# Optimization experiments

Measured on AMD Instinct MI355X. Metric: run time of the kernel, lower is better.

Reference implementation:

```python
import jax, jax.numpy as jnp
import numpy as np

NUM_POSES = 4096
NUM_PATCHES = 262144
NUM_OBS = 2097152


def setup_inputs() -> dict:
    key = jax.random.key(0)
    ks = jax.random.split(key, 7)
    poses = jax.random.normal(ks[0], (NUM_POSES, 7), dtype=jnp.float32)
    patch_coords = jax.random.normal(ks[1], (NUM_PATCHES, 2), dtype=jnp.float32)
    elevation_angle = jax.random.normal(ks[2], (NUM_PATCHES, 1), dtype=jnp.float32)
    poses_idx = jax.random.randint(ks[3], (NUM_OBS,), 0, NUM_POSES)
    patch_idx = jax.random.randint(ks[4], (NUM_OBS,), 0, NUM_PATCHES)
    target_coords = jax.random.normal(ks[5], (NUM_OBS, 3), dtype=jnp.float32)
    weights = jax.random.uniform(ks[6], (NUM_OBS, 1), dtype=jnp.float32)
    return {
        "poses": poses,
        "patch_coords": patch_coords,
        "elevation_angle": elevation_angle,
        "poses_idx": poses_idx,
        "patch_idx": patch_idx,
        "target_coords": target_coords,
        "weights": weights,
    }


def _se3_apply(pose7, pts):
    # pose7: [M,7] = (tx,ty,tz,qx,qy,qz,qw); pts: [M,3]
    # Equivalent to transform_matrix(pose) @ [pts; 1] (rotation by unit quaternion + translation)
    t = pose7[:, :3]
    q = pose7[:, 3:]
    q = q / jnp.linalg.norm(q, axis=-1, keepdims=True)  # pp.SE3 keeps unit quats
    qv, qw = q[:, :3], q[:, 3:4]
    uv = jnp.cross(qv, pts)                     # [M,3]
    rotated = pts + 2.0 * (qw * uv + jnp.cross(qv, uv))
    return rotated + t


def _cart2polar(xyz):
    # (x,y,z) -> (range, azimuth, elevation)
    x, y, z = xyz[:, 0], xyz[:, 1], xyz[:, 2]
    rho = jnp.sqrt(x * x + y * y)
    r = jnp.sqrt(rho * rho + z * z)
    az = jnp.arctan2(y, x)
    el = jnp.arctan2(z, rho)
    return jnp.stack([r, az, el], axis=1)


def reference(poses, patch_coords, elevation_angle, poses_idx, patch_idx, target_coords, weights):
    p = poses[poses_idx]                                            # [M,7] gather
    pts = jnp.concatenate(
        [patch_coords[patch_idx], elevation_angle[patch_idx]], axis=1
    )                                                               # [M,3] gather+cat
    proj = _cart2polar(_se3_apply(p, pts))                          # [M,3]
    residual = (proj - target_coords) * weights                     # [M,3]
    return residual
```

## Files before the change

kernel.cpp:

```cpp
#include <hip/hip_runtime.h>
#include <hip/hip_bf16.h>


__global__ __launch_bounds__(256) void ba_residual_kernel(
    const float* __restrict__ poses,
    const float* __restrict__ patch_coords,
    const float* __restrict__ elev,
    const int*   __restrict__ poses_idx,
    const int*   __restrict__ patch_idx,
    const float* __restrict__ target,
    const float* __restrict__ weights,
    float*       __restrict__ out,
    int n4)
{
    int i4 = blockIdx.x * blockDim.x + threadIdx.x;
    if (i4 >= n4) return;

    int4   pidx = reinterpret_cast<const int4*>(poses_idx)[i4];
    int4   qidx = reinterpret_cast<const int4*>(patch_idx)[i4];
    float4 w4   = reinterpret_cast<const float4*>(weights)[i4];
    float4 t0   = reinterpret_cast<const float4*>(target)[i4 * 3 + 0];
    float4 t1   = reinterpret_cast<const float4*>(target)[i4 * 3 + 1];
    float4 t2   = reinterpret_cast<const float4*>(target)[i4 * 3 + 2];

    int   pi[4] = {pidx.x, pidx.y, pidx.z, pidx.w};
    int   qi[4] = {qidx.x, qidx.y, qidx.z, qidx.w};
    float ww[4] = {w4.x, w4.y, w4.z, w4.w};
    float tg[12] = {t0.x, t0.y, t0.z, t0.w,
                    t1.x, t1.y, t1.z, t1.w,
                    t2.x, t2.y, t2.z, t2.w};

    float res[12];

#pragma unroll
    for (int k = 0; k < 4; ++k) {
        const float* p = poses + (size_t)pi[k] * 7;
        float tx = p[0], ty = p[1], tz = p[2];
        float qx = p[3], qy = p[4], qz = p[5], qw = p[6];
        float inv = rsqrtf(qx*qx + qy*qy + qz*qz + qw*qw);
        qx *= inv; qy *= inv; qz *= inv; qw *= inv;

        float2 pc = *reinterpret_cast<const float2*>(patch_coords + (size_t)qi[k] * 2);
        float px = pc.x, py = pc.y, pz = elev[qi[k]];

        float ux = qy*pz - qz*py;
        float uy = qz*px - qx*pz;
        float uz = qx*py - qy*px;
        float cx = qy*uz - qz*uy;
        float cy = qz*ux - qx*uz;
        float cz = qx*uy - qy*ux;
        float rx = px + 2.0f*(qw*ux + cx) + tx;
        float ry = py + 2.0f*(qw*uy + cy) + ty;
        float rz = pz + 2.0f*(qw*uz + cz) + tz;

        float rho = sqrtf(rx*rx + ry*ry);
        float r   = sqrtf(rho*rho + rz*rz);
        float az  = atan2f(ry, rx);
        float el  = atan2f(rz, rho);

        res[k*3 + 0] = (r  - tg[k*3 + 0]) * ww[k];
        res[k*3 + 1] = (az - tg[k*3 + 1]) * ww[k];
        res[k*3 + 2] = (el - tg[k*3 + 2]) * ww[k];
    }

    float4* o = reinterpret_cast<float4*>(out);
    o[i4 * 3 + 0] = make_float4(res[0], res[1], res[2],  res[3]);
    o[i4 * 3 + 1] = make_float4(res[4], res[5], res[6],  res[7]);
    o[i4 * 3 + 2] = make_float4(res[8], res[9], res[10], res[11]);
}

extern "C" void kernel_launch(void* const* d_in, const int* in_sizes, int n_in,
                              void* d_out, int out_size, void* d_ws, size_t ws_size,
                              hipStream_t stream) {
    const float* poses        = (const float*)d_in[0];
    const float* patch_coords = (const float*)d_in[1];
    const float* elev         = (const float*)d_in[2];
    const int*   poses_idx    = (const int*)d_in[3];
    const int*   patch_idx    = (const int*)d_in[4];
    const float* target       = (const float*)d_in[5];
    const float* weights      = (const float*)d_in[6];
    float*       out          = (float*)d_out;

    int n  = in_sizes[3];
    int n4 = n / 4;
    int block = 256;
    int grid = (n4 + block - 1) / block;
    ba_residual_kernel<<<grid, block, 0, stream>>>(
        poses, patch_coords, elev, poses_idx, patch_idx, target, weights, out, n4);
}
```

Baseline: 48.04 us.

## Prepack poses and patches into aligned vec4 tables; use nontemporal streaming I/O

```diff
diff --git a/kernel.cpp b/kernel.cpp
--- a/kernel.cpp
+++ b/kernel.cpp
@@ -2,10 +2,38 @@
 #include <hip/hip_bf16.h>
 
 
-__global__ __launch_bounds__(256) void ba_residual_kernel(
-    const float* __restrict__ poses,
-    const float* __restrict__ patch_coords,
-    const float* __restrict__ elev,
+#define NPOSES   4096
+#define NPATCHES 262144
+
+typedef float fvec4 __attribute__((ext_vector_type(4)));
+typedef int   ivec4 __attribute__((ext_vector_type(4)));
+
+__global__ __launch_bounds__(256) void pack_poses_kernel(
+    const float* __restrict__ poses, fvec4* __restrict__ pose4, int n)
+{
+    int i = blockIdx.x * blockDim.x + threadIdx.x;
+    if (i >= n) return;
+    const float* p = poses + (size_t)i * 7;
+    float tx = p[0], ty = p[1], tz = p[2];
+    float qx = p[3], qy = p[4], qz = p[5], qw = p[6];
+    float inv = rsqrtf(qx*qx + qy*qy + qz*qz + qw*qw);
+    pose4[2*i + 0] = (fvec4){tx, ty, tz, qw * inv};
+    pose4[2*i + 1] = (fvec4){qx * inv, qy * inv, qz * inv, 0.0f};
+}
+
+__global__ __launch_bounds__(256) void pack_patches_kernel(
+    const float* __restrict__ patch_coords, const float* __restrict__ elev,
+    fvec4* __restrict__ patch4, int n)
+{
+    int i = blockIdx.x * blockDim.x + threadIdx.x;
+    if (i >= n) return;
+    float2 pc = *reinterpret_cast<const float2*>(patch_coords + (size_t)i * 2);
+    patch4[i] = (fvec4){pc.x, pc.y, elev[i], 0.0f};
+}
+
+__global__ __launch_bounds__(256) void ba_main_kernel(
+    const fvec4* __restrict__ pose4,
+    const fvec4* __restrict__ patch4,
     const int*   __restrict__ poses_idx,
     const int*   __restrict__ patch_idx,
     const float* __restrict__ target,
@@ -16,12 +44,13 @@
     int i4 = blockIdx.x * blockDim.x + threadIdx.x;
     if (i4 >= n4) return;
 
-    int4   pidx = reinterpret_cast<const int4*>(poses_idx)[i4];
-    int4   qidx = reinterpret_cast<const int4*>(patch_idx)[i4];
-    float4 w4   = reinterpret_cast<const float4*>(weights)[i4];
-    float4 t0   = reinterpret_cast<const float4*>(target)[i4 * 3 + 0];
-    float4 t1   = reinterpret_cast<const float4*>(target)[i4 * 3 + 1];
-    float4 t2   = reinterpret_cast<const float4*>(target)[i4 * 3 + 2];
+    ivec4 pidx = __builtin_nontemporal_load(reinterpret_cast<const ivec4*>(poses_idx) + i4);
+    ivec4 qidx = __builtin_nontemporal_load(reinterpret_cast<const ivec4*>(patch_idx) + i4);
+    fvec4 w4   = __builtin_nontemporal_load(reinterpret_cast<const fvec4*>(weights) + i4);
+    const fvec4* tg4 = reinterpret_cast<const fvec4*>(target) + (size_t)i4 * 3;
+    fvec4 t0 = __builtin_nontemporal_load(tg4 + 0);
+    fvec4 t1 = __builtin_nontemporal_load(tg4 + 1);
+    fvec4 t2 = __builtin_nontemporal_load(tg4 + 2);
 
     int   pi[4] = {pidx.x, pidx.y, pidx.z, pidx.w};
     int   qi[4] = {qidx.x, qidx.y, qidx.z, qidx.w};
@@ -34,14 +63,12 @@
 
 #pragma unroll
     for (int k = 0; k < 4; ++k) {
-        const float* p = poses + (size_t)pi[k] * 7;
-        float tx = p[0], ty = p[1], tz = p[2];
-        float qx = p[3], qy = p[4], qz = p[5], qw = p[6];
-        float inv = rsqrtf(qx*qx + qy*qy + qz*qz + qw*qw);
-        qx *= inv; qy *= inv; qz *= inv; qw *= inv;
+        fvec4 pa = pose4[2*pi[k] + 0];
+        fvec4 pb = pose4[2*pi[k] + 1];
+        fvec4 pp = patch4[qi[k]];
 
-        float2 pc = *reinterpret_cast<const float2*>(patch_coords + (size_t)qi[k] * 2);
-        float px = pc.x, py = pc.y, pz = elev[qi[k]];
+        float qx = pb.x, qy = pb.y, qz = pb.z, qw = pa.w;
+        float px = pp.x, py = pp.y, pz = pp.z;
 
         float ux = qy*pz - qz*py;
         float uy = qz*px - qx*pz;
@@ -49,9 +76,9 @@
         float cx = qy*uz - qz*uy;
         float cy = qz*ux - qx*uz;
         float cz = qx*uy - qy*ux;
-        float rx = px + 2.0f*(qw*ux + cx) + tx;
-        float ry = py + 2.0f*(qw*uy + cy) + ty;
-        float rz = pz + 2.0f*(qw*uz + cz) + tz;
+        float rx = px + 2.0f*(qw*ux + cx) + pa.x;
+        float ry = py + 2.0f*(qw*uy + cy) + pa.y;
+        float rz = pz + 2.0f*(qw*uz + cz) + pa.z;
 
         float rho = sqrtf(rx*rx + ry*ry);
         float r   = sqrtf(rho*rho + rz*rz);
@@ -63,10 +90,42 @@
         res[k*3 + 2] = (el - tg[k*3 + 2]) * ww[k];
     }
 
-    float4* o = reinterpret_cast<float4*>(out);
-    o[i4 * 3 + 0] = make_float4(res[0], res[1], res[2],  res[3]);
-    o[i4 * 3 + 1] = make_float4(res[4], res[5], res[6],  res[7]);
-    o[i4 * 3 + 2] = make_float4(res[8], res[9], res[10], res[11]);
+    fvec4* o = reinterpret_cast<fvec4*>(out) + (size_t)i4 * 3;
+    __builtin_nontemporal_store((fvec4){res[0], res[1], res[2],  res[3]},  o + 0);
+    __builtin_nontemporal_store((fvec4){res[4], res[5], res[6],  res[7]},  o + 1);
+    __builtin_nontemporal_store((fvec4){res[8], res[9], res[10], res[11]}, o + 2);
+}
+
+__global__ __launch_bounds__(256) void ba_fallback_kernel(
+    const float* __restrict__ poses, const float* __restrict__ patch_coords,
+    const float* __restrict__ elev, const int* __restrict__ poses_idx,
+    const int* __restrict__ patch_idx, const float* __restrict__ target,
+    const float* __restrict__ weights, float* __restrict__ out, int n)
+{
+    int i = blockIdx.x * blockDim.x + threadIdx.x;
+    if (i >= n) return;
+    int pi = poses_idx[i];
+    int qi = patch_idx[i];
+    const float* p = poses + (size_t)pi * 7;
+    float tx = p[0], ty = p[1], tz = p[2];
+    float qx = p[3], qy = p[4], qz = p[5], qw = p[6];
+    float inv = rsqrtf(qx*qx + qy*qy + qz*qz + qw*qw);
+    qx *= inv; qy *= inv; qz *= inv; qw *= inv;
+    float2 pc = *reinterpret_cast<const float2*>(patch_coords + (size_t)qi * 2);
+    float px = pc.x, py = pc.y, pz = elev[qi];
+    float ux = qy*pz - qz*py, uy = qz*px - qx*pz, uz = qx*py - qy*px;
+    float cx = qy*uz - qz*uy, cy = qz*ux - qx*uz, cz = qx*uy - qy*ux;
+    float rx = px + 2.0f*(qw*ux + cx) + tx;
+    float ry = py + 2.0f*(qw*uy + cy) + ty;
+    float rz = pz + 2.0f*(qw*uz + cz) + tz;
+    float rho = sqrtf(rx*rx + ry*ry);
+    float r   = sqrtf(rho*rho + rz*rz);
+    float az  = atan2f(ry, rx);
+    float el  = atan2f(rz, rho);
+    float w = weights[i];
+    out[(size_t)i*3+0] = (r  - target[(size_t)i*3+0]) * w;
+    out[(size_t)i*3+1] = (az - target[(size_t)i*3+1]) * w;
+    out[(size_t)i*3+2] = (el - target[(size_t)i*3+2]) * w;
 }
 
 extern "C" void kernel_launch(void* const* d_in, const int* in_sizes, int n_in,
@@ -81,10 +140,23 @@
     const float* weights      = (const float*)d_in[6];
     float*       out          = (float*)d_out;
 
-    int n  = in_sizes[3];
-    int n4 = n / 4;
-    int block = 256;
-    int grid = (n4 + block - 1) / block;
-    ba_residual_kernel<<<grid, block, 0, stream>>>(
-        poses, patch_coords, elev, poses_idx, patch_idx, target, weights, out, n4);
+    int n = in_sizes[3];
+
+    size_t patch_bytes = (size_t)NPATCHES * 16;
+    size_t pose_bytes  = (size_t)NPOSES * 32;
+    if (ws_size >= patch_bytes + pose_bytes) {
+        fvec4* patch4 = (fvec4*)d_ws;
+        fvec4* pose4  = (fvec4*)((char*)d_ws + patch_bytes);
+
+        pack_poses_kernel<<<(NPOSES + 255) / 256, 256, 0, stream>>>(poses, pose4, NPOSES);
+        pack_patches_kernel<<<(NPATCHES + 255) / 256, 256, 0, stream>>>(
+            patch_coords, elev, patch4, NPATCHES);
+
+        int n4 = n / 4;
+        ba_main_kernel<<<(n4 + 255) / 256, 256, 0, stream>>>(
+            pose4, patch4, poses_idx, patch_idx, target, weights, out, n4);
+    } else {
+        ba_fallback_kernel<<<(n + 255) / 256, 256, 0, stream>>>(
+            poses, patch_coords, elev, poses_idx, patch_idx, target, weights, out, n);
+    }
 }
```

Measured after the change: 58.93 us. 1.23x slower.
